# Kernel tuning notes

Measured on AMD Instinct MI355X. Metric: run time of the kernel, lower is better.

## Reference

```python
import jax, jax.numpy as jnp
import numpy as np

EPS = 1e-12  # matches torch F.normalize default eps


def setup_inputs() -> dict:
    key = jax.random.key(0)
    k1, k2 = jax.random.split(key)
    x = jax.random.normal(k1, (64, 256, 32, 32), dtype=jnp.float32)
    prototype_bank = jax.random.normal(k2, (512, 256), dtype=jnp.float32)
    return {"x": x, "prototype_bank": prototype_bank}


def reference(x, prototype_bank):
    B, C, H, W = x.shape
    HW = H * W
    xf = x.reshape(B, C, HW)
    # L2-normalize over channel dim (dim=1), torch F.normalize semantics
    xn = xf / jnp.maximum(jnp.linalg.norm(xf, axis=1, keepdims=True), EPS)
    pn = prototype_bank / jnp.maximum(
        jnp.linalg.norm(prototype_bank, axis=1, keepdims=True), EPS)
    # cosine similarities: (B, HW, P) -- fused matmul instead of broadcast multiply-sum
    sims = jnp.einsum('bcn,pc->bnp', xn, pn)
    indices = jnp.argmax(sims, axis=2)  # (B, HW), int
    # gather UNnormalized prototypes, then reshape (B*HW, C) -> (B, H, W, C) -> (B, C, H, W)
    recon = prototype_bank[indices.reshape(-1)]  # (B*HW, C)
    recon = recon.reshape(B, H, W, C).transpose(0, 3, 1, 2)
    return recon, indices
```

## Files before the change

kernel.cpp:

```cpp
#include <hip/hip_runtime.h>
#include <hip/hip_bf16.h>

typedef __attribute__((ext_vector_type(8))) short short8;
typedef __attribute__((ext_vector_type(4))) float f32x4;

#define NPOS  65536
#define NOUT  16777216
#define QCAP  384
#define DELTA 0.05f

__global__ __launch_bounds__(256) void proto_prep(
    const float* __restrict__ proto, float* __restrict__ pnN,
    ushort* __restrict__ pnBF) {
  int p = blockIdx.x;
  int c = threadIdx.x;
  float v = proto[p * 256 + c];
  float s = v * v;
  #pragma unroll
  for (int off = 32; off > 0; off >>= 1) s += __shfl_down(s, off);
  __shared__ float red[4];
  int lane = c & 63, wid = c >> 6;
  if (lane == 0) red[wid] = s;
  __syncthreads();
  float tot = red[0] + red[1] + red[2] + red[3];
  float nrm = fmaxf(sqrtf(tot), 1e-12f);
  float q = v / nrm;
  pnN[p * 256 + c] = q;
  __hip_bfloat16 h = __float2bfloat16(q);
  pnBF[p * 256 + c] = *reinterpret_cast<ushort*>(&h);
}

__global__ __launch_bounds__(512, 4) void match_kernel(
    const float* __restrict__ x, const float* __restrict__ proto,
    const float* __restrict__ pnN, const ushort* __restrict__ pnBF,
    float* __restrict__ out) {
  __shared__ __align__(16) float  raw[128 * 64];
  __shared__ __align__(16) ushort xbf[64 * 256];
  __shared__ float wmax[8][64];
  __shared__ float thr[64];
  __shared__ int   queue[QCAP];
  __shared__ float qscore[QCAP];
  __shared__ int   idxl[64];
  __shared__ int   qn;

  const int t = threadIdx.x;
  const int l = t & 63, w = t >> 6;
  const int g = l >> 4, r8 = l & 7, c16 = l & 15;
  const int n0 = blockIdx.x << 6;
  const int b = n0 >> 10, hw0 = n0 & 1023;
  const float* xg = x + ((size_t)b << 18) + hw0;

  if (t == 0) qn = 0;

  for (int ph = 0; ph < 2; ++ph) {
    __syncthreads();
    #pragma unroll
    for (int i = 0; i < 4; ++i) {
      int q = t + (i << 9);
      int krel = q >> 4, m4 = (q & 15) << 2;
      const float4* src =
          reinterpret_cast<const float4*>(xg + (((ph << 7) + krel) << 10) + m4);
      *reinterpret_cast<float4*>(&raw[(krel << 6) + m4]) = *src;
    }
    __syncthreads();
    #pragma unroll
    for (int i = 0; i < 2; ++i) {
      int q = t + (i << 9);
      int m = q & 63, cR = q >> 6;
      short8 pk;
      #pragma unroll
      for (int j = 0; j < 8; ++j) {
        float v = raw[(((cR << 3) + j) << 6) + m];
        __hip_bfloat16 h = __float2bfloat16(v);
        pk[j] = *reinterpret_cast<short*>(&h);
      }
      int chunk = (ph << 4) + cR;
      int dst = (m << 8) + ((chunk ^ (m & 7)) << 3);
      *reinterpret_cast<short8*>(&xbf[dst]) = pk;
    }
  }
  __syncthreads();

  const ushort* pB0 = pnBF + (((w << 6) + c16) << 8) + (g << 3);
  f32x4 acc[4][4];
  #pragma unroll
  for (int mi = 0; mi < 4; ++mi)
    #pragma unroll
    for (int ni = 0; ni < 4; ++ni) acc[mi][ni] = (f32x4){0.f, 0.f, 0.f, 0.f};

  short8 Bcur[4], Bnxt[4];
  #pragma unroll
  for (int ni = 0; ni < 4; ++ni)
    Bcur[ni] = *reinterpret_cast<const short8*>(pB0 + (ni << 12));

  #pragma unroll
  for (int ks = 0; ks < 8; ++ks) {
    if (ks < 7) {
      #pragma unroll
      for (int ni = 0; ni < 4; ++ni)
        Bnxt[ni] = *reinterpret_cast<const short8*>(pB0 + (ni << 12) + ((ks + 1) << 5));
    }
    #pragma unroll
    for (int mi = 0; mi < 4; ++mi) {
      int chunk = (ks << 2) + g;
      const short8 a = *reinterpret_cast<const short8*>(
          &xbf[(((mi << 4) + c16) << 8) + ((chunk ^ r8) << 3)]);
      #pragma unroll
      for (int ni = 0; ni < 4; ++ni)
        acc[mi][ni] =
            __builtin_amdgcn_mfma_f32_16x16x32_bf16(a, Bcur[ni], acc[mi][ni], 0, 0, 0);
    }
    if (ks < 7) {
      #pragma unroll
      for (int ni = 0; ni < 4; ++ni) Bcur[ni] = Bnxt[ni];
    }
  }

  #pragma unroll
  for (int mi = 0; mi < 4; ++mi) {
    #pragma unroll
    for (int r = 0; r < 4; ++r) {
      float v = fmaxf(fmaxf(acc[mi][0][r], acc[mi][1][r]),
                      fmaxf(acc[mi][2][r], acc[mi][3][r]));
      #pragma unroll
      for (int s = 1; s < 16; s <<= 1) v = fmaxf(v, __shfl_xor(v, s));
      if (c16 == 0) wmax[w][(mi << 4) + (g << 2) + r] = v;
    }
  }
  __syncthreads();
  if (t < 64) {
    float bm = wmax[0][t];
    #pragma unroll
    for (int ww = 1; ww < 8; ++ww) bm = fmaxf(bm, wmax[ww][t]);
    thr[t] = bm - DELTA;
  }
  __syncthreads();

  #pragma unroll
  for (int mi = 0; mi < 4; ++mi)
    #pragma unroll
    for (int ni = 0; ni < 4; ++ni)
      #pragma unroll
      for (int r = 0; r < 4; ++r) {
        int pos = (mi << 4) + (g << 2) + r;
        if (acc[mi][ni][r] >= thr[pos]) {
          int slot = atomicAdd(&qn, 1);
          if (slot < QCAP)
            queue[slot] = ((((w << 6) + (ni << 4) + c16)) << 6) | pos;
        }
      }
  __syncthreads();

  int n = qn < QCAP ? qn : QCAP;
  for (int j = t; j < n; j += 512) {
    int e = queue[j];
    int pos = e & 63, p = e >> 6;
    float a = 0.f;
    const float* pr = pnN + (p << 8);
    for (int k = 0; k < 256; ++k)
      a = fmaf(xg[(k << 10) + pos], pr[k], a);
    qscore[j] = a;
  }
  __syncthreads();

  if (t < 64) {
    float best = -3.4e38f;
    int bp = 1 << 30;
    for (int j = 0; j < n; ++j) {
      if ((queue[j] & 63) == t) {
        float s = qscore[j];
        int p = queue[j] >> 6;
        if (s > best || (s == best && p < bp)) { best = s; bp = p; }
      }
    }
    idxl[t] = bp;
    out[(size_t)NOUT + n0 + t] = (float)bp;
  }
  __syncthreads();

  float* rb = out + ((size_t)b << 18) + hw0;
  #pragma unroll 1
  for (int it = 0; it < 32; ++it) {
    int lin = (it << 9) + t;
    int c = lin >> 6, pos = lin & 63;
    rb[((size_t)c << 10) + pos] = proto[(idxl[pos] << 8) + c];
  }
}

extern "C" void kernel_launch(void* const* d_in, const int* in_sizes, int n_in,
                              void* d_out, int out_size, void* d_ws, size_t ws_size,
                              hipStream_t stream) {
  const float* x = (const float*)d_in[0];
  const float* proto = (const float*)d_in[1];
  float* out = (float*)d_out;
  float* pnN = (float*)d_ws;
  ushort* pnBF = (ushort*)((char*)d_ws + 512 * 256 * sizeof(float));

  proto_prep<<<512, 256, 0, stream>>>(proto, pnN, pnBF);
  match_kernel<<<NPOS / 64, 512, 0, stream>>>(x, proto, pnN, pnBF, out);
}
```

Before: 119.4 us.

## Shrink LDS and registers to double occupancy with direct-to-LDS loads

Swaps the raw staging buffer for a small one shared through a union with the queue and scratch arrays. x is now loaded in eight small phases using global_load_lds direct-to-LDS copies. The GEMM accumulators go from 16 tiles to 4 by looping over four 16-row M chunks, each with its own threshold and queue pass, and launch bounds rise to 8 blocks per SM. The goal is higher occupancy to hide memory latency. The cost is many more barriers, B fragments re-read from global memory on every M chunk with no prefetch, and a smaller queue capacity that could overflow and change results.

```diff
diff --git a/kernel.cpp b/kernel.cpp
--- a/kernel.cpp
+++ b/kernel.cpp
@@ -2,11 +2,12 @@
 #include <hip/hip_bf16.h>
 
 typedef __attribute__((ext_vector_type(8))) short short8;
+typedef __attribute__((ext_vector_type(4))) short short4v;
 typedef __attribute__((ext_vector_type(4))) float f32x4;
 
 #define NPOS  65536
 #define NOUT  16777216
-#define QCAP  384
+#define QCAP  240
 #define DELTA 0.05f
 
 __global__ __launch_bounds__(256) void proto_prep(
@@ -30,136 +31,118 @@
   pnBF[p * 256 + c] = *reinterpret_cast<ushort*>(&h);
 }
 
-__global__ __launch_bounds__(512, 4) void match_kernel(
+__global__ __launch_bounds__(512, 8) void match_kernel(
     const float* __restrict__ x, const float* __restrict__ proto,
     const float* __restrict__ pnN, const ushort* __restrict__ pnBF,
     float* __restrict__ out) {
-  __shared__ __align__(16) float  raw[128 * 64];
   __shared__ __align__(16) ushort xbf[64 * 256];
-  __shared__ float wmax[8][64];
-  __shared__ float thr[64];
-  __shared__ int   queue[QCAP];
-  __shared__ float qscore[QCAP];
-  __shared__ int   idxl[64];
-  __shared__ int   qn;
+  __shared__ __align__(16) union UU {
+    float raw[32 * 64];
+    struct {
+      float wmax[8][16];
+      float thr[16];
+      int   queue[QCAP];
+      float qscore[QCAP];
+      int   idxl[64];
+      int   qn;
+    } s;
+  } u;
 
   const int t = threadIdx.x;
   const int l = t & 63, w = t >> 6;
-  const int g = l >> 4, r8 = l & 7, c16 = l & 15;
+  const int g = l >> 4, c16 = l & 15, r8 = l & 7;
   const int n0 = blockIdx.x << 6;
   const int b = n0 >> 10, hw0 = n0 & 1023;
   const float* xg = x + ((size_t)b << 18) + hw0;
 
-  if (t == 0) qn = 0;
-
-  for (int ph = 0; ph < 2; ++ph) {
-    __syncthreads();
-    #pragma unroll
-    for (int i = 0; i < 4; ++i) {
-      int q = t + (i << 9);
-      int krel = q >> 4, m4 = (q & 15) << 2;
-      const float4* src =
-          reinterpret_cast<const float4*>(xg + (((ph << 7) + krel) << 10) + m4);
-      *reinterpret_cast<float4*>(&raw[(krel << 6) + m4]) = *src;
+  #pragma unroll 1
+  for (int p = 0; p < 8; ++p) {
+    {
+      const float* src =
+          xg + ((((p << 5) + (w << 2) + (l >> 4)) << 10)) + ((l & 15) << 2);
+      float* dst = &u.raw[w << 8];
+      __builtin_amdgcn_global_load_lds(
+          (const __attribute__((address_space(1))) unsigned int*)src,
+          (__attribute__((address_space(3))) unsigned int*)dst, 16, 0, 0);
     }
     __syncthreads();
-    #pragma unroll
-    for (int i = 0; i < 2; ++i) {
-      int q = t + (i << 9);
-      int m = q & 63, cR = q >> 6;
-      short8 pk;
+    {
+      int m = t & 63, c4 = t >> 6;
+      short4v q;
       #pragma unroll
-      for (int j = 0; j < 8; ++j) {
-        float v = raw[(((cR << 3) + j) << 6) + m];
+      for (int j = 0; j < 4; ++j) {
+        float v = u.raw[(((c4 << 2) + j) << 6) + m];
         __hip_bfloat16 h = __float2bfloat16(v);
-        pk[j] = *reinterpret_cast<short*>(&h);
+        q[j] = *reinterpret_cast<short*>(&h);
       }
-      int chunk = (ph << 4) + cR;
-      int dst = (m << 8) + ((chunk ^ (m & 7)) << 3);
-      *reinterpret_cast<short8*>(&xbf[dst]) = pk;
+      int chunk = (p << 2) + (c4 >> 1);
+      int dst = (m << 8) + ((chunk ^ (m & 7)) << 3) + ((c4 & 1) << 2);
+      *reinterpret_cast<short4v*>(&xbf[dst]) = q;
     }
+    __syncthreads();
   }
-  __syncthreads();
+
+  if (t == 0) u.s.qn = 0;
 
   const ushort* pB0 = pnBF + (((w << 6) + c16) << 8) + (g << 3);
-  f32x4 acc[4][4];
-  #pragma unroll
-  for (int mi = 0; mi < 4; ++mi)
+
+  #pragma unroll 1
+  for (int mq = 0; mq < 4; ++mq) {
+    f32x4 acc[4];
     #pragma unroll
-    for (int ni = 0; ni < 4; ++ni) acc[mi][ni] = (f32x4){0.f, 0.f, 0.f, 0.f};
+    for (int ni = 0; ni < 4; ++ni) acc[ni] = (f32x4){0.f, 0.f, 0.f, 0.f};
 
-  short8 Bcur[4], Bnxt[4];
-  #pragma unroll
-  for (int ni = 0; ni < 4; ++ni)
-    Bcur[ni] = *reinterpret_cast<const short8*>(pB0 + (ni << 12));
+    #pragma unroll
+    for (int ks = 0; ks < 8; ++ks) {
+      const short8 a = *reinterpret_cast<const short8*>(
+          &xbf[(((mq << 4) + c16) << 8) + ((((ks << 2) + g) ^ r8) << 3)]);
+      #pragma unroll
+      for (int ni = 0; ni < 4; ++ni) {
+        const short8 bf = *reinterpret_cast<const short8*>(
+            pB0 + (ni << 12) + (ks << 5));
+        acc[ni] = __builtin_amdgcn_mfma_f32_16x16x32_bf16(a, bf, acc[ni], 0, 0, 0);
+      }
+    }
 
-  #pragma unroll
-  for (int ks = 0; ks < 8; ++ks) {
-    if (ks < 7) {
-      #pragma unroll
-      for (int ni = 0; ni < 4; ++ni)
-        Bnxt[ni] = *reinterpret_cast<const short8*>(pB0 + (ni << 12) + ((ks + 1) << 5));
-    }
-    #pragma unroll
-    for (int mi = 0; mi < 4; ++mi) {
-      int chunk = (ks << 2) + g;
-      const short8 a = *reinterpret_cast<const short8*>(
-          &xbf[(((mi << 4) + c16) << 8) + ((chunk ^ r8) << 3)]);
-      #pragma unroll
-      for (int ni = 0; ni < 4; ++ni)
-        acc[mi][ni] =
-            __builtin_amdgcn_mfma_f32_16x16x32_bf16(a, Bcur[ni], acc[mi][ni], 0, 0, 0);
-    }
-    if (ks < 7) {
-      #pragma unroll
-      for (int ni = 0; ni < 4; ++ni) Bcur[ni] = Bnxt[ni];
-    }
-  }
-
-  #pragma unroll
-  for (int mi = 0; mi < 4; ++mi) {
     #pragma unroll
     for (int r = 0; r < 4; ++r) {
-      float v = fmaxf(fmaxf(acc[mi][0][r], acc[mi][1][r]),
-                      fmaxf(acc[mi][2][r], acc[mi][3][r]));
+      float v = fmaxf(fmaxf(acc[0][r], acc[1][r]), fmaxf(acc[2][r], acc[3][r]));
       #pragma unroll
       for (int s = 1; s < 16; s <<= 1) v = fmaxf(v, __shfl_xor(v, s));
-      if (c16 == 0) wmax[w][(mi << 4) + (g << 2) + r] = v;
+      if (c16 == 0) u.s.wmax[w][(g << 2) + r] = v;
     }
-  }
-  __syncthreads();
-  if (t < 64) {
-    float bm = wmax[0][t];
-    #pragma unroll
-    for (int ww = 1; ww < 8; ++ww) bm = fmaxf(bm, wmax[ww][t]);
-    thr[t] = bm - DELTA;
-  }
-  __syncthreads();
-
-  #pragma unroll
-  for (int mi = 0; mi < 4; ++mi)
+    __syncthreads();
+    if (t < 16) {
+      float bm = u.s.wmax[0][t];
+      #pragma unroll
+      for (int ww = 1; ww < 8; ++ww) bm = fmaxf(bm, u.s.wmax[ww][t]);
+      u.s.thr[t] = bm - DELTA;
+    }
+    __syncthreads();
     #pragma unroll
     for (int ni = 0; ni < 4; ++ni)
       #pragma unroll
       for (int r = 0; r < 4; ++r) {
-        int pos = (mi << 4) + (g << 2) + r;
-        if (acc[mi][ni][r] >= thr[pos]) {
-          int slot = atomicAdd(&qn, 1);
+        int p16 = (g << 2) + r;
+        if (acc[ni][r] >= u.s.thr[p16]) {
+          int slot = atomicAdd(&u.s.qn, 1);
           if (slot < QCAP)
-            queue[slot] = ((((w << 6) + (ni << 4) + c16)) << 6) | pos;
+            u.s.queue[slot] =
+                (((w << 6) + (ni << 4) + c16) << 6) | ((mq << 4) + p16);
         }
       }
-  __syncthreads();
+    __syncthreads();
+  }
 
-  int n = qn < QCAP ? qn : QCAP;
+  int n = u.s.qn < QCAP ? u.s.qn : QCAP;
   for (int j = t; j < n; j += 512) {
-    int e = queue[j];
+    int e = u.s.queue[j];
     int pos = e & 63, p = e >> 6;
     float a = 0.f;
     const float* pr = pnN + (p << 8);
     for (int k = 0; k < 256; ++k)
       a = fmaf(xg[(k << 10) + pos], pr[k], a);
-    qscore[j] = a;
+    u.s.qscore[j] = a;
   }
   __syncthreads();
 
@@ -167,13 +150,13 @@
     float best = -3.4e38f;
     int bp = 1 << 30;
     for (int j = 0; j < n; ++j) {
-      if ((queue[j] & 63) == t) {
-        float s = qscore[j];
-        int p = queue[j] >> 6;
+      if ((u.s.queue[j] & 63) == t) {
+        float s = u.s.qscore[j];
+        int p = u.s.queue[j] >> 6;
         if (s > best || (s == best && p < bp)) { best = s; bp = p; }
       }
     }
-    idxl[t] = bp;
+    u.s.idxl[t] = bp;
     out[(size_t)NOUT + n0 + t] = (float)bp;
   }
   __syncthreads();
@@ -183,7 +166,7 @@
   for (int it = 0; it < 32; ++it) {
     int lin = (it << 9) + t;
     int c = lin >> 6, pos = lin & 63;
-    rb[((size_t)c << 10) + pos] = proto[(idxl[pos] << 8) + c];
+    rb[((size_t)c << 10) + pos] = proto[(u.s.idxl[pos] << 8) + c];
   }
 }
 
```

Measured after the change: 271.8 us. +127.7%, slower.
